# Optimization experiments

Measured on AMD Instinct MI355X. Metric: run time of the kernel, lower is better.

Reference implementation:

```python
import jax, jax.numpy as jnp
import numpy as np

DIM = 256
NUM_HEADS = 8

def setup_inputs() -> dict:
    key = jax.random.key(0)
    ks = jax.random.split(key, 5)
    x = jax.random.normal(ks[0], (2, 4096, DIM), dtype=jnp.float32)
    s = 1.0 / np.sqrt(DIM)
    W_qkv = jax.random.normal(ks[1], (DIM, 3 * DIM), dtype=jnp.float32) * s
    b_qkv = jax.random.normal(ks[2], (3 * DIM,), dtype=jnp.float32) * 0.02
    W_proj = jax.random.normal(ks[3], (DIM, DIM), dtype=jnp.float32) * s
    b_proj = jax.random.normal(ks[4], (DIM,), dtype=jnp.float32) * 0.02
    return {"x": x, "W_qkv": W_qkv, "b_qkv": b_qkv, "W_proj": W_proj, "b_proj": b_proj}

def reference(x, W_qkv, b_qkv, W_proj, b_proj):
    B, N, C = x.shape
    H = NUM_HEADS
    Dh = C // H
    scale = C ** (-0.5)  # NOTE: original scales by full dim, not head_dim
    qkv = (x @ W_qkv + b_qkv).reshape(B, N, 3, H, Dh)
    q, k, v = jnp.moveaxis(qkv, 2, 0)  # each [B, N, H, Dh]
    q = q.transpose(0, 2, 1, 3)  # [B, H, N, Dh]
    k = k.transpose(0, 2, 1, 3)
    v = v.transpose(0, 2, 1, 3)
    attn = jnp.einsum('bhnd,bhmd->bhnm', q, k) * scale
    attn = jax.nn.softmax(attn, axis=-1)
    out = jnp.einsum('bhnm,bhmd->bhnd', attn, v)
    out = out.transpose(0, 2, 1, 3).reshape(B, N, C)
    return out @ W_proj + b_proj
```

## Files before the change

kernel.cpp:

```cpp
#include <hip/hip_runtime.h>

#define NSEQ 4096
#define BATCH 2
#define ROWS (BATCH * NSEQ)
#define NH 8
#define DHD 32

typedef __attribute__((ext_vector_type(8))) short bf16x8;
typedef __attribute__((ext_vector_type(4))) float f32x4;

static __device__ __forceinline__ ushort f2bf(float f) {
    union { float f; uint u; } v; v.f = f;
    uint u = v.u;
    uint r = (u + 0x7fffu + ((u >> 16) & 1u)) >> 16;
    return (ushort)r;
}

__global__ __launch_bounds__(256) void k_prep(const float* __restrict__ x,
                                              ushort* __restrict__ xb,
                                              const float* __restrict__ wqkv,
                                              const float* __restrict__ wproj,
                                              ushort* __restrict__ wqkvT,
                                              ushort* __restrict__ wprojT) {
    __shared__ float tile[32][33];
    int bid = blockIdx.x;
    if (bid < 2048) {
        int i = (bid * 256 + threadIdx.x) * 4;
        float4 v = *(const float4*)(x + i);
        ushort4 o;
        o.x = f2bf(v.x); o.y = f2bf(v.y); o.z = f2bf(v.z); o.w = f2bf(v.w);
        *(ushort4*)(xb + i) = o;
        return;
    }
    int tb = bid - 2048;
    int nt = tb & 31, kt = tb >> 5;
    const float* src; ushort* dst; int ncols, nbase;
    if (nt < 24) { src = wqkv;  dst = wqkvT;  ncols = 768; nbase = nt * 32; }
    else         { src = wproj; dst = wprojT; ncols = 256; nbase = (nt - 24) * 32; }
    int tx = threadIdx.x & 31, ty = threadIdx.x >> 5;
#pragma unroll
    for (int j = 0; j < 4; ++j)
        tile[ty + j * 8][tx] = src[(size_t)(kt * 32 + ty + j * 8) * ncols + nbase + tx];
    __syncthreads();
#pragma unroll
    for (int j = 0; j < 4; ++j)
        dst[(size_t)(nbase + ty + j * 8) * 256 + kt * 32 + tx] = f2bf(tile[tx][ty + j * 8]);
}

__global__ __launch_bounds__(256) void k_qkv(const ushort* __restrict__ xb,
                                             const ushort* __restrict__ wt,
                                             const float* __restrict__ bias,
                                             ushort* __restrict__ qh,
                                             ushort* __restrict__ kh,
                                             ushort* __restrict__ vT) {
    __shared__ __align__(16) ushort Al[64][264];
    __shared__ __align__(16) ushort Bl[64][264];
    int t = threadIdx.x;
    int w = t >> 6, lane = t & 63;
    int lhi = lane >> 4, llo = lane & 15;
    int row0 = blockIdx.x * 64;
    int n0 = blockIdx.y * 64;

#pragma unroll
    for (int j = 0; j < 8; ++j) {
        int f = j * 256 + t;
        int r = f >> 5, c = (f & 31) * 8;
        *(bf16x8*)&Al[r][c] = *(const bf16x8*)(xb + (size_t)(row0 + r) * 256 + c);
        *(bf16x8*)&Bl[r][c] = *(const bf16x8*)(wt + (size_t)(n0 + r) * 256 + c);
    }
    __syncthreads();

    f32x4 acc[4] = {};
#pragma unroll
    for (int ks = 0; ks < 8; ++ks) {
        int k0 = ks * 32 + lhi * 8;
        bf16x8 a = *(const bf16x8*)&Al[w * 16 + llo][k0];
#pragma unroll
        for (int fn = 0; fn < 4; ++fn) {
            bf16x8 b = *(const bf16x8*)&Bl[fn * 16 + llo][k0];
            acc[fn] = __builtin_amdgcn_mfma_f32_16x16x32_bf16(a, b, acc[fn], 0, 0, 0);
        }
    }

    int bb = row0 >> 12;
    int nb = row0 & 4095;
    if (blockIdx.y < 8) {
#pragma unroll
        for (int fn = 0; fn < 4; ++fn) {
            int cg = n0 + fn * 16 + llo;
            int three = cg >> 8, rem = cg & 255;
            int hh = rem >> 5, dh = rem & 31;
            float bv = bias[cg];
            size_t hb = (size_t)(bb * NH + hh);
#pragma unroll
            for (int r = 0; r < 4; ++r) {
                int n = nb + w * 16 + lhi * 4 + r;
                float v = acc[fn][r] + bv;
                if (three == 0) qh[(hb * 4096 + (size_t)n) * 32 + dh] = f2bf(v * 0.0625f);
                else            kh[(hb * 4096 + (size_t)n) * 32 + dh] = f2bf(v);
            }
        }
    } else {
        __syncthreads();
        ushort (*vbuf)[68] = (ushort(*)[68])&Al[0][0];
#pragma unroll
        for (int fn = 0; fn < 4; ++fn) {
            int c = fn * 16 + llo;
            float bv = bias[n0 + c];
#pragma unroll
            for (int r = 0; r < 4; ++r) {
                int s = w * 16 + lhi * 4 + r;
                int np = ((s >> 5) << 5) | (((s & 15) >> 2) << 3)
                       | (((s >> 4) & 1) << 2) | (s & 3);
                vbuf[c][np] = f2bf(acc[fn][r] + bv);
            }
        }
        __syncthreads();
#pragma unroll
        for (int j = 0; j < 2; ++j) {
            int f = j * 256 + t;
            int col = f >> 3, ch = (f & 7) * 8;
            bf16x8 val = *(const bf16x8*)&vbuf[col][ch];
            int dh = col & 31;
            int hh = ((int)blockIdx.y - 8) * 2 + (col >> 5);
            size_t hb = (size_t)(bb * NH + hh);
            *(bf16x8*)(vT + (hb * DHD + dh) * NSEQ + nb + ch) = val;
        }
    }
}

__global__ __launch_bounds__(256) void k_attn(const ushort* __restrict__ qh,
                                              const ushort* __restrict__ kh,
                                              const ushort* __restrict__ vT,
                                              ushort* __restrict__ attn_out) {
    __shared__ __align__(16) ushort Klds[4][64][40];
    __shared__ __align__(16) ushort Vlds[4][32][72];
    int t = threadIdx.x;
    int w = t >> 6, lane = t & 63;
    int lhi = lane >> 4, llo = lane & 15;
    int xcd = blockIdx.x & 7, qp = blockIdx.x >> 3;
    int bh = xcd * 2 + (qp >> 6);
    int qblk = qp & 63;
    int b = bh >> 3, h = bh & 7;
    int q0 = qblk * 64 + w * 16;

    const ushort* qbase = qh + (size_t)bh * 4096 * 32;
    const ushort* kg = kh + (size_t)bh * 4096 * 32 + (t >> 2) * 32 + (t & 3) * 8;
    const ushort* vg = vT + (size_t)bh * 32 * 4096 + (t >> 3) * 4096 + (t & 7) * 8;
    ushort* klp = &Klds[0][t >> 2][(t & 3) * 8];
    ushort* vlp = &Vlds[0][t >> 3][(t & 7) * 8];
    const int KLB = 64 * 40, VLB = 32 * 72;

    bf16x8 qf = *(const bf16x8*)(qbase + (q0 + llo) * 32 + lhi * 8);
    short onebits = (llo == 0) ? (short)0x3F80 : (short)0;
    bf16x8 va2 = {onebits, onebits, onebits, onebits, onebits, onebits, onebits, onebits};

    f32x4 acc0 = {}, acc1 = {}, acc2 = {};
    const float L2E = 1.4426950408889634f;
    float mrun = 0.f, nmL2E = 0.f, mthr = 8.f;
    const f32x4 zf = {0.f, 0.f, 0.f, 0.f};

    auto COMPUTE = [&](int cur) {
        const ushort* Kb = &Klds[cur][0][0];
        const ushort* Vb = &Vlds[cur][0][0];
        bf16x8 k0 = *(const bf16x8*)(Kb + (llo) * 40 + lhi * 8);
        bf16x8 k1 = *(const bf16x8*)(Kb + (16 + llo) * 40 + lhi * 8);
        bf16x8 k2 = *(const bf16x8*)(Kb + (32 + llo) * 40 + lhi * 8);
        bf16x8 k3 = *(const bf16x8*)(Kb + (48 + llo) * 40 + lhi * 8);
        bf16x8 v00 = *(const bf16x8*)(Vb + llo * 72 + lhi * 8);
        bf16x8 v01 = *(const bf16x8*)(Vb + (llo + 16) * 72 + lhi * 8);
        bf16x8 v10 = *(const bf16x8*)(Vb + llo * 72 + 32 + lhi * 8);
        bf16x8 v11 = *(const bf16x8*)(Vb + (llo + 16) * 72 + 32 + lhi * 8);
        __builtin_amdgcn_s_setprio(1);
        f32x4 sf0 = __builtin_amdgcn_mfma_f32_16x16x32_bf16(k0, qf, zf, 0, 0, 0);
        f32x4 sf1 = __builtin_amdgcn_mfma_f32_16x16x32_bf16(k1, qf, zf, 0, 0, 0);
        f32x4 sf2 = __builtin_amdgcn_mfma_f32_16x16x32_bf16(k2, qf, zf, 0, 0, 0);
        f32x4 sf3 = __builtin_amdgcn_mfma_f32_16x16x32_bf16(k3, qf, zf, 0, 0, 0);
        __builtin_amdgcn_s_setprio(0);
        float g0 = fmaxf(fmaxf(sf0[0], sf0[1]), sf0[2]);
        float g1 = fmaxf(fmaxf(sf0[3], sf1[0]), sf1[1]);
        float g2 = fmaxf(fmaxf(sf1[2], sf1[3]), sf2[0]);
        float g3 = fmaxf(fmaxf(sf2[1], sf2[2]), sf2[3]);
        float g4 = fmaxf(fmaxf(sf3[0], sf3[1]), sf3[2]);
        float h0 = fmaxf(fmaxf(g0, g1), g2);
        float h1 = fmaxf(fmaxf(g3, g4), sf3[3]);
        float tm = fmaxf(h0, h1);
        if (!__all(tm <= mthr)) {
            float rmax = fmaxf(tm, __shfl_xor(tm, 16));
            rmax = fmaxf(rmax, __shfl_xor(rmax, 32));
            float mnew = fmaxf(mrun, rmax);
            float corr = __builtin_amdgcn_exp2f((mrun - mnew) * L2E);
            mrun = mnew; nmL2E = -mrun * L2E; mthr = mrun + 8.f;
#pragma unroll
            for (int r = 0; r < 4; ++r) {
                float fc = __shfl(corr, lhi * 4 + r);
                acc0[r] *= fc; acc1[r] *= fc; acc2[r] *= fc;
            }
        }
        float e00 = __builtin_amdgcn_exp2f(__builtin_fmaf(sf0[0], L2E, nmL2E));
        float e01 = __builtin_amdgcn_exp2f(__builtin_fmaf(sf0[1], L2E, nmL2E));
        float e02 = __builtin_amdgcn_exp2f(__builtin_fmaf(sf0[2], L2E, nmL2E));
        float e03 = __builtin_amdgcn_exp2f(__builtin_fmaf(sf0[3], L2E, nmL2E));
        float e10 = __builtin_amdgcn_exp2f(__builtin_fmaf(sf1[0], L2E, nmL2E));
        float e11 = __builtin_amdgcn_exp2f(__builtin_fmaf(sf1[1], L2E, nmL2E));
        float e12 = __builtin_amdgcn_exp2f(__builtin_fmaf(sf1[2], L2E, nmL2E));
        float e13 = __builtin_amdgcn_exp2f(__builtin_fmaf(sf1[3], L2E, nmL2E));
        float e20 = __builtin_amdgcn_exp2f(__builtin_fmaf(sf2[0], L2E, nmL2E));
        float e21 = __builtin_amdgcn_exp2f(__builtin_fmaf(sf2[1], L2E, nmL2E));
        float e22 = __builtin_amdgcn_exp2f(__builtin_fmaf(sf2[2], L2E, nmL2E));
        float e23 = __builtin_amdgcn_exp2f(__builtin_fmaf(sf2[3], L2E, nmL2E));
        float e30 = __builtin_amdgcn_exp2f(__builtin_fmaf(sf3[0], L2E, nmL2E));
        float e31 = __builtin_amdgcn_exp2f(__builtin_fmaf(sf3[1], L2E, nmL2E));
        float e32 = __builtin_amdgcn_exp2f(__builtin_fmaf(sf3[2], L2E, nmL2E));
        float e33 = __builtin_amdgcn_exp2f(__builtin_fmaf(sf3[3], L2E, nmL2E));
        union PU { uint u[4]; bf16x8 v; };
        PU pa0, pa1;
        asm("v_cvt_pk_bf16_f32 %0, %1, %2" : "=v"(pa0.u[0]) : "v"(e00), "v"(e01));
        asm("v_cvt_pk_bf16_f32 %0, %1, %2" : "=v"(pa0.u[1]) : "v"(e02), "v"(e03));
        asm("v_cvt_pk_bf16_f32 %0, %1, %2" : "=v"(pa0.u[2]) : "v"(e10), "v"(e11));
        asm("v_cvt_pk_bf16_f32 %0, %1, %2" : "=v"(pa0.u[3]) : "v"(e12), "v"(e13));
        asm("v_cvt_pk_bf16_f32 %0, %1, %2" : "=v"(pa1.u[0]) : "v"(e20), "v"(e21));
        asm("v_cvt_pk_bf16_f32 %0, %1, %2" : "=v"(pa1.u[1]) : "v"(e22), "v"(e23));
        asm("v_cvt_pk_bf16_f32 %0, %1, %2" : "=v"(pa1.u[2]) : "v"(e30), "v"(e31));
        asm("v_cvt_pk_bf16_f32 %0, %1, %2" : "=v"(pa1.u[3]) : "v"(e32), "v"(e33));
        __builtin_amdgcn_s_setprio(1);
        acc0 = __builtin_amdgcn_mfma_f32_16x16x32_bf16(pa0.v, v00, acc0, 0, 0, 0);
        acc1 = __builtin_amdgcn_mfma_f32_16x16x32_bf16(pa0.v, v01, acc1, 0, 0, 0);
        acc2 = __builtin_amdgcn_mfma_f32_16x16x32_bf16(pa0.v, va2, acc2, 0, 0, 0);
        acc0 = __builtin_amdgcn_mfma_f32_16x16x32_bf16(pa1.v, v10, acc0, 0, 0, 0);
        acc1 = __builtin_amdgcn_mfma_f32_16x16x32_bf16(pa1.v, v11, acc1, 0, 0, 0);
        acc2 = __builtin_amdgcn_mfma_f32_16x16x32_bf16(pa1.v, va2, acc2, 0, 0, 0);
        __builtin_amdgcn_s_setprio(0);
    };

    {
        bf16x8 k0t = *(const bf16x8*)(kg);
        bf16x8 v0t = *(const bf16x8*)(vg);
        bf16x8 k1t = *(const bf16x8*)(kg + 2048);
        bf16x8 v1t = *(const bf16x8*)(vg + 64);
        *(bf16x8*)(klp) = k0t;
        *(bf16x8*)(vlp) = v0t;
        *(bf16x8*)(klp + KLB) = k1t;
        *(bf16x8*)(vlp + VLB) = v1t;
    }
    __syncthreads();
    bf16x8 kA = *(const bf16x8*)(kg + 2 * 2048);
    bf16x8 vA = *(const bf16x8*)(vg + 2 * 64);
    bf16x8 kB = *(const bf16x8*)(kg + 3 * 2048);
    bf16x8 vB = *(const bf16x8*)(vg + 3 * 64);

#pragma unroll 1
    for (int ip = 0; ip < 16; ++ip) {
        *(bf16x8*)(klp + 2 * KLB) = kA;
        *(bf16x8*)(vlp + 2 * VLB) = vA;
        *(bf16x8*)(klp + 3 * KLB) = kB;
        *(bf16x8*)(vlp + 3 * VLB) = vB;
        if (ip < 15) {
            kA = *(const bf16x8*)(kg + (size_t)(4 * ip + 4) * 2048);
            vA = *(const bf16x8*)(vg + (4 * ip + 4) * 64);
            kB = *(const bf16x8*)(kg + (size_t)(4 * ip + 5) * 2048);
            vB = *(const bf16x8*)(vg + (4 * ip + 5) * 64);
        }
        COMPUTE(0);
        COMPUTE(1);
        __syncthreads();
        if (ip < 15) {
            *(bf16x8*)(klp) = kA;
            *(bf16x8*)(vlp) = vA;
            *(bf16x8*)(klp + KLB) = kB;
            *(bf16x8*)(vlp + VLB) = vB;
            kA = *(const bf16x8*)(kg + (size_t)(4 * ip + 6) * 2048);
            vA = *(const bf16x8*)(vg + (4 * ip + 6) * 64);
            kB = *(const bf16x8*)(kg + (size_t)(4 * ip + 7) * 2048);
            vB = *(const bf16x8*)(vg + (4 * ip + 7) * 64);
        }
        COMPUTE(2);
        COMPUTE(3);
        __syncthreads();
    }

#pragma unroll
    for (int r = 0; r < 4; ++r) {
        float ls = __shfl(acc2[r], lhi * 16);
        float li = 1.f / ls;
        int row = q0 + lhi * 4 + r;
        size_t orow = ((size_t)(b * NSEQ) + row) * 256 + h * DHD;
        attn_out[orow + llo] = f2bf(acc0[r] * li);
        attn_out[orow + 16 + llo] = f2bf(acc1[r] * li);
    }
}

__global__ __launch_bounds__(256) void k_proj(const ushort* __restrict__ aout,
                                              const ushort* __restrict__ wt,
                                              const float* __restrict__ bias,
                                              float* __restrict__ out) {
    __shared__ __align__(16) ushort Al[64][264];
    __shared__ __align__(16) ushort Bl[64][264];
    int t = threadIdx.x;
    int w = t >> 6, lane = t & 63;
    int lhi = lane >> 4, llo = lane & 15;
    int row0 = blockIdx.x * 64;
    int n0 = blockIdx.y * 64;

#pragma unroll
    for (int j = 0; j < 8; ++j) {
        int f = j * 256 + t;
        int r = f >> 5, c = (f & 31) * 8;
        *(bf16x8*)&Al[r][c] = *(const bf16x8*)(aout + (size_t)(row0 + r) * 256 + c);
        *(bf16x8*)&Bl[r][c] = *(const bf16x8*)(wt + (size_t)(n0 + r) * 256 + c);
    }
    __syncthreads();

    f32x4 acc[4] = {};
#pragma unroll
    for (int ks = 0; ks < 8; ++ks) {
        int k0 = ks * 32 + lhi * 8;
        bf16x8 a = *(const bf16x8*)&Al[w * 16 + llo][k0];
#pragma unroll
        for (int fn = 0; fn < 4; ++fn) {
            bf16x8 b = *(const bf16x8*)&Bl[fn * 16 + llo][k0];
            acc[fn] = __builtin_amdgcn_mfma_f32_16x16x32_bf16(a, b, acc[fn], 0, 0, 0);
        }
    }
#pragma unroll
    for (int fn = 0; fn < 4; ++fn) {
        int cg = n0 + fn * 16 + llo;
        float bv = bias[cg];
#pragma unroll
        for (int r = 0; r < 4; ++r) {
            int row = row0 + w * 16 + lhi * 4 + r;
            out[(size_t)row * 256 + cg] = acc[fn][r] + bv;
        }
    }
}

extern "C" void kernel_launch(void* const* d_in, const int* in_sizes, int n_in,
                              void* d_out, int out_size, void* d_ws, size_t ws_size,
                              hipStream_t stream) {
    const float* x     = (const float*)d_in[0];
    const float* Wqkv  = (const float*)d_in[1];
    const float* bqkv  = (const float*)d_in[2];
    const float* Wproj = (const float*)d_in[3];
    const float* bproj = (const float*)d_in[4];
    float* out = (float*)d_out;

    char* ws = (char*)d_ws;
    ushort* xb     = (ushort*)(ws);
    ushort* wqkvT  = (ushort*)(ws + 4194304);
    ushort* wprojT = (ushort*)(ws + 4587520);
    ushort* qhb    = (ushort*)(ws + 4718592);
    ushort* khb    = (ushort*)(ws + 8912896);
    ushort* vT     = (ushort*)(ws + 13107200);
    ushort* aoutb  = (ushort*)(ws + 17301504);

    k_prep<<<2304, 256, 0, stream>>>(x, xb, Wqkv, Wproj, wqkvT, wprojT);
    k_qkv<<<dim3(128, 12), 256, 0, stream>>>(xb, wqkvT, bqkv, qhb, khb, vT);
    k_attn<<<1024, 256, 0, stream>>>(qhb, khb, vT, aoutb);
    k_proj<<<dim3(128, 4), 256, 0, stream>>>(aoutb, wprojT, bproj, out);
}
```

Before: 94.15 us.

## Load K fragments directly from global into registers, bypassing LDS

Removes the K staging buffer in shared memory. Each wave now loads its K MFMA fragments straight from global memory into registers, prefetching the next tile one step ahead inside the compute lambda. This drops the LDS write and read traffic for K and shrinks the shared-memory footprint. The cost is that every wave in the block re-reads the same K tile from global memory or cache (four times the global loads), adds register pressure, and exposes global latency with only one tile of prefetch lead.

```diff
diff --git a/kernel.cpp b/kernel.cpp
--- a/kernel.cpp
+++ b/kernel.cpp
@@ -133,7 +133,6 @@
                                               const ushort* __restrict__ kh,
                                               const ushort* __restrict__ vT,
                                               ushort* __restrict__ attn_out) {
-    __shared__ __align__(16) ushort Klds[4][64][40];
     __shared__ __align__(16) ushort Vlds[4][32][72];
     int t = threadIdx.x;
     int w = t >> 6, lane = t & 63;
@@ -145,11 +144,10 @@
     int q0 = qblk * 64 + w * 16;
 
     const ushort* qbase = qh + (size_t)bh * 4096 * 32;
-    const ushort* kg = kh + (size_t)bh * 4096 * 32 + (t >> 2) * 32 + (t & 3) * 8;
+    const ushort* kf0 = kh + (size_t)bh * 4096 * 32 + llo * 32 + lhi * 8;
     const ushort* vg = vT + (size_t)bh * 32 * 4096 + (t >> 3) * 4096 + (t & 7) * 8;
-    ushort* klp = &Klds[0][t >> 2][(t & 3) * 8];
     ushort* vlp = &Vlds[0][t >> 3][(t & 7) * 8];
-    const int KLB = 64 * 40, VLB = 32 * 72;
+    const int VLB = 32 * 72;
 
     bf16x8 qf = *(const bf16x8*)(qbase + (q0 + llo) * 32 + lhi * 8);
     short onebits = (llo == 0) ? (short)0x3F80 : (short)0;
@@ -160,22 +158,28 @@
     float mrun = 0.f, nmL2E = 0.f, mthr = 8.f;
     const f32x4 zf = {0.f, 0.f, 0.f, 0.f};
 
-    auto COMPUTE = [&](int cur) {
-        const ushort* Kb = &Klds[cur][0][0];
-        const ushort* Vb = &Vlds[cur][0][0];
-        bf16x8 k0 = *(const bf16x8*)(Kb + (llo) * 40 + lhi * 8);
-        bf16x8 k1 = *(const bf16x8*)(Kb + (16 + llo) * 40 + lhi * 8);
-        bf16x8 k2 = *(const bf16x8*)(Kb + (32 + llo) * 40 + lhi * 8);
-        bf16x8 k3 = *(const bf16x8*)(Kb + (48 + llo) * 40 + lhi * 8);
+    bf16x8 kC0, kC1, kC2, kC3;
+
+    auto COMPUTE = [&](int vb, int ti) {
+        const ushort* Vb = &Vlds[vb][0][0];
         bf16x8 v00 = *(const bf16x8*)(Vb + llo * 72 + lhi * 8);
         bf16x8 v01 = *(const bf16x8*)(Vb + (llo + 16) * 72 + lhi * 8);
         bf16x8 v10 = *(const bf16x8*)(Vb + llo * 72 + 32 + lhi * 8);
         bf16x8 v11 = *(const bf16x8*)(Vb + (llo + 16) * 72 + 32 + lhi * 8);
+        bf16x8 kn0, kn1, kn2, kn3;
+        bool pf = (ti + 1 < 64);
+        if (pf) {
+            const ushort* kp = kf0 + (size_t)(ti + 1) * 2048;
+            kn0 = *(const bf16x8*)(kp);
+            kn1 = *(const bf16x8*)(kp + 512);
+            kn2 = *(const bf16x8*)(kp + 1024);
+            kn3 = *(const bf16x8*)(kp + 1536);
+        }
         __builtin_amdgcn_s_setprio(1);
-        f32x4 sf0 = __builtin_amdgcn_mfma_f32_16x16x32_bf16(k0, qf, zf, 0, 0, 0);
-        f32x4 sf1 = __builtin_amdgcn_mfma_f32_16x16x32_bf16(k1, qf, zf, 0, 0, 0);
-        f32x4 sf2 = __builtin_amdgcn_mfma_f32_16x16x32_bf16(k2, qf, zf, 0, 0, 0);
-        f32x4 sf3 = __builtin_amdgcn_mfma_f32_16x16x32_bf16(k3, qf, zf, 0, 0, 0);
+        f32x4 sf0 = __builtin_amdgcn_mfma_f32_16x16x32_bf16(kC0, qf, zf, 0, 0, 0);
+        f32x4 sf1 = __builtin_amdgcn_mfma_f32_16x16x32_bf16(kC1, qf, zf, 0, 0, 0);
+        f32x4 sf2 = __builtin_amdgcn_mfma_f32_16x16x32_bf16(kC2, qf, zf, 0, 0, 0);
+        f32x4 sf3 = __builtin_amdgcn_mfma_f32_16x16x32_bf16(kC3, qf, zf, 0, 0, 0);
         __builtin_amdgcn_s_setprio(0);
         float g0 = fmaxf(fmaxf(sf0[0], sf0[1]), sf0[2]);
         float g1 = fmaxf(fmaxf(sf0[3], sf1[0]), sf1[1]);
@@ -231,51 +235,42 @@
         acc1 = __builtin_amdgcn_mfma_f32_16x16x32_bf16(pa1.v, v11, acc1, 0, 0, 0);
         acc2 = __builtin_amdgcn_mfma_f32_16x16x32_bf16(pa1.v, va2, acc2, 0, 0, 0);
         __builtin_amdgcn_s_setprio(0);
+        if (pf) { kC0 = kn0; kC1 = kn1; kC2 = kn2; kC3 = kn3; }
     };
 
     {
-        bf16x8 k0t = *(const bf16x8*)(kg);
         bf16x8 v0t = *(const bf16x8*)(vg);
-        bf16x8 k1t = *(const bf16x8*)(kg + 2048);
         bf16x8 v1t = *(const bf16x8*)(vg + 64);
-        *(bf16x8*)(klp) = k0t;
         *(bf16x8*)(vlp) = v0t;
-        *(bf16x8*)(klp + KLB) = k1t;
         *(bf16x8*)(vlp + VLB) = v1t;
     }
+    kC0 = *(const bf16x8*)(kf0);
+    kC1 = *(const bf16x8*)(kf0 + 512);
+    kC2 = *(const bf16x8*)(kf0 + 1024);
+    kC3 = *(const bf16x8*)(kf0 + 1536);
     __syncthreads();
-    bf16x8 kA = *(const bf16x8*)(kg + 2 * 2048);
     bf16x8 vA = *(const bf16x8*)(vg + 2 * 64);
-    bf16x8 kB = *(const bf16x8*)(kg + 3 * 2048);
     bf16x8 vB = *(const bf16x8*)(vg + 3 * 64);
 
 #pragma unroll 1
     for (int ip = 0; ip < 16; ++ip) {
-        *(bf16x8*)(klp + 2 * KLB) = kA;
         *(bf16x8*)(vlp + 2 * VLB) = vA;
-        *(bf16x8*)(klp + 3 * KLB) = kB;
         *(bf16x8*)(vlp + 3 * VLB) = vB;
         if (ip < 15) {
-            kA = *(const bf16x8*)(kg + (size_t)(4 * ip + 4) * 2048);
             vA = *(const bf16x8*)(vg + (4 * ip + 4) * 64);
-            kB = *(const bf16x8*)(kg + (size_t)(4 * ip + 5) * 2048);
             vB = *(const bf16x8*)(vg + (4 * ip + 5) * 64);
         }
-        COMPUTE(0);
-        COMPUTE(1);
+        COMPUTE(0, 4 * ip + 0);
+        COMPUTE(1, 4 * ip + 1);
         __syncthreads();
         if (ip < 15) {
-            *(bf16x8*)(klp) = kA;
             *(bf16x8*)(vlp) = vA;
-            *(bf16x8*)(klp + KLB) = kB;
             *(bf16x8*)(vlp + VLB) = vB;
-            kA = *(const bf16x8*)(kg + (size_t)(4 * ip + 6) * 2048);
             vA = *(const bf16x8*)(vg + (4 * ip + 6) * 64);
-            kB = *(const bf16x8*)(kg + (size_t)(4 * ip + 7) * 2048);
             vB = *(const bf16x8*)(vg + (4 * ip + 7) * 64);
         }
-        COMPUTE(2);
-        COMPUTE(3);
+        COMPUTE(2, 4 * ip + 2);
+        COMPUTE(3, 4 * ip + 3);
         __syncthreads();
     }
 
```

Result: slower. 107.1 us (+13.8%).
